# Optimization experiments

Hardware: AMD Instinct MI355X
Metric: run time of the kernel (lower is better)

Reference implementation:

```python
import jax, jax.numpy as jnp
import numpy as np

NUM_HEADS = 8
DIM = 256
NW = 64  # number of windows per batch element


def setup_inputs() -> dict:
    key = jax.random.key(0)
    k_x, k_m, k_ws, k_wm, k_wp, k_bp = jax.random.split(key, 6)
    B_, N, C = 512, 128, DIM
    x = jax.random.normal(k_x, (B_, N, C), dtype=jnp.float32)
    # 0 / -100 additive attention mask (stand-in for the 0/-inf shift-window mask)
    mask = jnp.where(jax.random.uniform(k_m, (NW, N, N)) < 0.5, 0.0, -100.0).astype(jnp.float32)
    std = 0.02
    w_qkv_self = jax.random.normal(k_ws, (3 * C, C), dtype=jnp.float32) * std
    w_qkv_mut = jax.random.normal(k_wm, (3 * C, C), dtype=jnp.float32) * std
    w_proj = jax.random.normal(k_wp, (C, 2 * C), dtype=jnp.float32) * std
    b_proj = jax.random.normal(k_bp, (C,), dtype=jnp.float32) * std
    return {"x": x, "mask": mask, "w_qkv_self": w_qkv_self,
            "w_qkv_mut": w_qkv_mut, "w_proj": w_proj, "b_proj": b_proj}


def _split_qkv(x, w):
    # x: (B_, N, C); w: (3C, C) torch Linear weight -> y = x @ w.T
    B_, N, C = x.shape
    d = C // NUM_HEADS
    qkv = (x @ w.T).reshape(B_, N, 3, NUM_HEADS, d).transpose(2, 0, 3, 1, 4)
    return qkv[0], qkv[1], qkv[2]  # each (B_, H, N, d)


def _attention(q, k, v, mask, scale):
    # q,k,v: (B_, H, n, d); mask: (nW, Nfull, Nfull) additive
    B_, H, n, d = q.shape
    nW = mask.shape[0]
    attn = jnp.einsum('bhnd,bhmd->bhnm', q * scale, k)  # (B_, H, n, n)
    attn = attn.reshape(B_ // nW, nW, H, n, n) + mask[None, :, None, :n, :n]
    attn = jax.nn.softmax(attn.reshape(B_, H, n, n), axis=-1)
    out = jnp.einsum('bhnm,bhmd->bhnd', attn, v)
    return out.transpose(0, 2, 1, 3).reshape(B_, n, H * d)  # (B_, n, C)


def reference(x, mask, w_qkv_self, w_qkv_mut, w_proj, b_proj):
    B_, N, C = x.shape
    scale = (C // NUM_HEADS) ** (-0.5)
    # self window attention
    q, k, v = _split_qkv(x, w_qkv_self)
    x_out = _attention(q, k, v, mask, scale)  # (B_, N, C)
    # mutual (cross-frame) attention between the two halves of the window
    qm, km, vm = _split_qkv(x, w_qkv_mut)
    h = N // 2
    q1, q2 = qm[:, :, :h], qm[:, :, h:]
    k1, k2 = km[:, :, :h], km[:, :, h:]
    v1, v2 = vm[:, :, :h], vm[:, :, h:]
    x1_aligned = _attention(q2, k1, v1, mask, scale)  # (B_, N//2, C)
    x2_aligned = _attention(q1, k2, v2, mask, scale)  # (B_, N//2, C)
    x_mut = jnp.concatenate([x1_aligned, x2_aligned], axis=1)  # (B_, N, C)
    x_cat = jnp.concatenate([x_mut, x_out], axis=2)  # (B_, N, 2C)
    return x_cat @ w_proj.T + b_proj  # (B_, N, C)
```

## Files before the change

### kernel.cpp

```cpp
#include <hip/hip_runtime.h>
#include <stdint.h>

typedef __bf16 bf16x4 __attribute__((ext_vector_type(4)));
typedef __bf16 bf16x8 __attribute__((ext_vector_type(8)));
typedef float f32x4 __attribute__((ext_vector_type(4)));

#define DEVI __device__ __forceinline__

DEVI ushort bfbits(float f) {
  union { __bf16 b; ushort u; } v;
  v.b = (__bf16)f;
  return v.u;
}

DEVI void gload16(const void* g, void* l) {
  auto* gp = reinterpret_cast<const __attribute__((address_space(1))) uint32_t*>(
      reinterpret_cast<uintptr_t>(g));
  auto* lp = reinterpret_cast<__attribute__((address_space(3))) uint32_t*>(
      reinterpret_cast<uintptr_t>(l));
  __builtin_amdgcn_global_load_lds(gp, lp, 16, 0, 0);
}

__global__ __launch_bounds__(256) void cvt_x(const float* __restrict__ in,
                                             ushort* __restrict__ out) {
  int i = (blockIdx.x * 256 + threadIdx.x) * 4;
  float4 v = *(const float4*)(in + i);
  ushort4 o;
  o.x = bfbits(v.x); o.y = bfbits(v.y); o.z = bfbits(v.z); o.w = bfbits(v.w);
  *(ushort4*)(out + i) = o;
}

__global__ __launch_bounds__(256) void cvt_w(const float* __restrict__ ws,
                                             const float* __restrict__ wm,
                                             const float* __restrict__ wp,
                                             ushort* __restrict__ wqkv,
                                             ushort* __restrict__ wproj) {
  int i = blockIdx.x * 256 + threadIdx.x;
  if (i < 196608)       wqkv[i] = bfbits(ws[i]);
  else if (i < 393216)  wqkv[i] = bfbits(wm[i - 196608]);
  else                  wproj[i - 393216] = bfbits(wp[i - 393216]);
}

template <int KF, int NH>
DEVI void attn_body(const ushort* Qs, const ushort* Ks, const ushort* Vt,
                    ushort* Ps, const float* mrow, ushort* ob,
                    int qrow0, int kvbase, int orow0, int mrow0,
                    int lr, int lc) {
  const float L2E = 1.4426950408889634f;

  f32x4 sacc[2][KF];
#pragma unroll
  for (int mf = 0; mf < 2; ++mf)
#pragma unroll
    for (int nf = 0; nf < KF; ++nf) sacc[mf][nf] = (f32x4){0.f, 0.f, 0.f, 0.f};

  bf16x8 aq[2];
#pragma unroll
  for (int mf = 0; mf < 2; ++mf) {
    int r = qrow0 + mf * 16 + lr;
    aq[mf] = *(const bf16x8*)(Qs + r * 32 + ((lc ^ ((r >> 1) & 3)) * 8));
  }
  __builtin_amdgcn_s_setprio(1);
#pragma unroll
  for (int nf = 0; nf < KF; ++nf) {
    int r = kvbase + nf * 16 + lr;
    bf16x8 bk = *(const bf16x8*)(Ks + r * 32 + ((lc ^ ((r >> 1) & 3)) * 8));
#pragma unroll
    for (int mf = 0; mf < 2; ++mf)
      sacc[mf][nf] = __builtin_amdgcn_mfma_f32_16x16x32_bf16(aq[mf], bk, sacc[mf][nf], 0, 0, 0);
  }
  __builtin_amdgcn_s_setprio(0);

#pragma unroll
  for (int mf = 0; mf < 2; ++mf)
#pragma unroll
    for (int nf = 0; nf < KF; ++nf)
#pragma unroll
      for (int r = 0; r < 4; ++r) {
        int row = mrow0 + mf * 16 + lc * 4 + r;
        int col = nf * 16 + lr;
        sacc[mf][nf][r] = fmaf(mrow[row * 128 + col], L2E, sacc[mf][nf][r]);
      }
  float sinv[2][4];
#pragma unroll
  for (int mf = 0; mf < 2; ++mf)
#pragma unroll
    for (int r = 0; r < 4; ++r) {
      float s = 0.f;
#pragma unroll
      for (int nf = 0; nf < KF; ++nf) {
        float e = __builtin_amdgcn_exp2f(sacc[mf][nf][r]);
        sacc[mf][nf][r] = e;
        s += e;
      }
#pragma unroll
      for (int d = 1; d < 16; d <<= 1) s += __shfl_xor(s, d);
      sinv[mf][r] = __builtin_amdgcn_rcpf(s);
    }

  f32x4 oacc[2][2];
#pragma unroll
  for (int mf = 0; mf < 2; ++mf)
#pragma unroll
    for (int nf = 0; nf < 2; ++nf) oacc[mf][nf] = (f32x4){0.f, 0.f, 0.f, 0.f};

#pragma unroll
  for (int hf = 0; hf < NH; ++hf) {
    __syncthreads();
#pragma unroll
    for (int mf = 0; mf < 2; ++mf)
#pragma unroll
      for (int r = 0; r < 4; ++r) {
        int prow = orow0 + mf * 16 + lc * 4 + r;
#pragma unroll
        for (int nf2 = 0; nf2 < 4; ++nf2) {
          int col = nf2 * 16 + lr;
          int grp = (col >> 3) ^ (prow & 7);
          Ps[prow * 64 + grp * 8 + (col & 7)] = bfbits(sacc[mf][hf * 4 + nf2][r]);
        }
      }
    __syncthreads();
    __builtin_amdgcn_s_setprio(1);
#pragma unroll
    for (int ks = 0; ks < 2; ++ks) {
      bf16x8 pf[2], vf[2];
#pragma unroll
      for (int mf = 0; mf < 2; ++mf) {
        int prow = orow0 + mf * 16 + lr;
        int grp = (ks * 4 + lc) ^ (prow & 7);
        pf[mf] = *(const bf16x8*)(Ps + prow * 64 + grp * 8);
      }
#pragma unroll
      for (int nf = 0; nf < 2; ++nf)
        vf[nf] = *(const bf16x8*)(Vt + (nf * 16 + lr) * 136 + kvbase + hf * 64 + ks * 32 + lc * 8);
#pragma unroll
      for (int mf = 0; mf < 2; ++mf)
#pragma unroll
        for (int nf = 0; nf < 2; ++nf)
          oacc[mf][nf] = __builtin_amdgcn_mfma_f32_16x16x32_bf16(pf[mf], vf[nf], oacc[mf][nf], 0, 0, 0);
    }
    __builtin_amdgcn_s_setprio(0);
  }

#pragma unroll
  for (int mf = 0; mf < 2; ++mf)
#pragma unroll
    for (int nf = 0; nf < 2; ++nf)
#pragma unroll
      for (int r = 0; r < 4; ++r) {
        int row = orow0 + mf * 16 + lc * 4 + r;
        int col = nf * 16 + lr;
        ob[(size_t)row * 512 + col] = bfbits(oacc[mf][nf][r] * sinv[mf][r]);
      }
}

__global__ __launch_bounds__(256) void attn_fused(const ushort* __restrict__ xb,
                                                  const ushort* __restrict__ wqkv,
                                                  const float* __restrict__ mask,
                                                  ushort* __restrict__ xcat) {
  __shared__ __align__(16) uint8_t smem[28672];
  ushort* xs0 = (ushort*)smem;
  ushort* wl0 = (ushort*)(smem + 8192);
  ushort* xs1 = (ushort*)(smem + 14336);
  ushort* wl1 = (ushort*)(smem + 22528);
  ushort* Qs  = (ushort*)smem;
  ushort* Ks  = (ushort*)(smem + 8192);
  ushort* Vt  = (ushort*)(smem + 16384);
  ushort* Ps  = (ushort*)smem;

  const int bid = blockIdx.x;
  const int c = bid & 7;
  const int u = bid >> 3;
  const int m = u & 1;
  const int h = (u >> 1) & 7;
  const int b = (u >> 4) * 8 + c;
  const int wmask = b & 63;
  const int t = threadIdx.x;
  const int wid = t >> 6, l = t & 63;
  const int lr = l & 15, lc = l >> 4;
  const float qscale = 0.17677669529663687f * 1.4426950408889634f;

  const ushort* xrow = xb + (size_t)b * 128 * 256;
  const int wbase = m * 768;

  auto STAGE = [&](int kk, ushort* xs, ushort* wl) {
#pragma unroll
    for (int p = 0; p < 2; ++p) {
      int slot = t + p * 256;
      int row = slot >> 2, cs = slot & 3;
      int cd = cs ^ ((row >> 1) & 3);
      gload16(xrow + (size_t)row * 256 + kk + cd * 8, xs + slot * 8);
    }
    {
      int slot = t;
      int row = slot >> 2, cs = slot & 3;
      int cd = cs ^ ((row >> 1) & 3);
      int grow = wbase + (row >> 5) * 256 + h * 32 + (row & 31);
      gload16(wqkv + (size_t)grow * 256 + kk + cd * 8, wl + slot * 8);
    }
    if (t < 128) {
      int slot = t + 256;
      int row = slot >> 2, cs = slot & 3;
      int cd = cs ^ ((row >> 1) & 3);
      int grow = wbase + (row >> 5) * 256 + h * 32 + (row & 31);
      gload16(wqkv + (size_t)grow * 256 + kk + cd * 8, wl + slot * 8);
    }
  };

  f32x4 pacc[2][6];
#pragma unroll
  for (int mf = 0; mf < 2; ++mf)
#pragma unroll
    for (int n = 0; n < 6; ++n) pacc[mf][n] = (f32x4){0.f, 0.f, 0.f, 0.f};

  STAGE(0, xs0, wl0);
#pragma unroll
  for (int k = 0; k < 8; ++k) {
    __syncthreads();
    if (k < 7) {
      if ((k & 1) == 0) STAGE((k + 1) * 32, xs1, wl1);
      else              STAGE((k + 1) * 32, xs0, wl0);
    }
    const ushort* xs = (k & 1) ? xs1 : xs0;
    const ushort* wl = (k & 1) ? wl1 : wl0;

    bf16x8 ax[2];
#pragma unroll
    for (int mf = 0; mf < 2; ++mf) {
      int r = wid * 32 + mf * 16 + lr;
      ax[mf] = *(const bf16x8*)(xs + r * 32 + ((lc ^ ((r >> 1) & 3)) * 8));
    }
    __builtin_amdgcn_s_setprio(1);
#pragma unroll
    for (int n = 0; n < 6; ++n) {
      int r = n * 16 + lr;
      bf16x8 bw = *(const bf16x8*)(wl + r * 32 + ((lc ^ ((r >> 1) & 3)) * 8));
#pragma unroll
      for (int mf = 0; mf < 2; ++mf)
        pacc[mf][n] = __builtin_amdgcn_mfma_f32_16x16x32_bf16(ax[mf], bw, pacc[mf][n], 0, 0, 0);
    }
    __builtin_amdgcn_s_setprio(0);
  }
  __syncthreads();

#pragma unroll
  for (int mf = 0; mf < 2; ++mf) {
#pragma unroll
    for (int n = 0; n < 4; ++n)
#pragma unroll
      for (int j = 0; j < 4; ++j) {
        int row = wid * 32 + mf * 16 + lc * 4 + j;
        int d = (n & 1) * 16 + lr;
        float v = pacc[mf][n][j];
        if (n < 2) v *= qscale;
        int sw = ((d >> 3) ^ ((row >> 1) & 3)) * 8 + (d & 7);
        (n < 2 ? Qs : Ks)[row * 32 + sw] = bfbits(v);
      }
#pragma unroll
    for (int k = 0; k < 2; ++k) {
      bf16x4 pk;
#pragma unroll
      for (int j = 0; j < 4; ++j) pk[j] = (__bf16)pacc[mf][4 + k][j];
      int d = k * 16 + lr;
      int row0 = wid * 32 + mf * 16 + lc * 4;
      *(bf16x4*)(Vt + d * 136 + row0) = pk;
    }
  }
  __syncthreads();

  const float* mrow = mask + (size_t)wmask * 16384;

  if (m == 0) {
    ushort* ob = xcat + (size_t)b * 128 * 512 + 256 + h * 32;
    attn_body<8, 2>(Qs, Ks, Vt, Ps, mrow, ob,
                    wid * 32, 0,
                    wid * 32, wid * 32, lr, lc);
  } else {
    const int half = wid >> 1, sub = wid & 1;
    ushort* ob = xcat + (size_t)b * 128 * 512 + h * 32;
    attn_body<4, 1>(Qs, Ks, Vt, Ps, mrow, ob,
                    (half ? 0 : 64) + sub * 32, half ? 64 : 0,
                    half * 64 + sub * 32, sub * 32, lr, lc);
  }
}

__global__ __launch_bounds__(256) void gemm_proj(const ushort* __restrict__ A,
                                                 const ushort* __restrict__ B,
                                                 const float* __restrict__ bias,
                                                 float* __restrict__ out) {
  __shared__ ushort As[64 * 32];
  __shared__ ushort Bs[256 * 32];
  const int t = threadIdx.x, tm = blockIdx.x;
  const int w = t >> 6, l = t & 63;
  const int wc = w * 64;
  const int lr = l & 15, lc = l >> 4;
  const ushort* Ab = A + (size_t)tm * 64 * 512;

  f32x4 acc[4][4];
#pragma unroll
  for (int m = 0; m < 4; ++m)
#pragma unroll
    for (int n = 0; n < 4; ++n) acc[m][n] = (f32x4){0.f, 0.f, 0.f, 0.f};

  for (int kk = 0; kk < 512; kk += 32) {
    __syncthreads();
    {
      int slot = t;
      int row = slot >> 2, cs = slot & 3;
      int cd = cs ^ ((row >> 1) & 3);
      gload16(Ab + (size_t)row * 512 + kk + cd * 8, As + slot * 8);
    }
#pragma unroll
    for (int p = 0; p < 4; ++p) {
      int slot = t + p * 256;
      int row = slot >> 2, cs = slot & 3;
      int cd = cs ^ ((row >> 1) & 3);
      gload16(B + (size_t)row * 512 + kk + cd * 8, Bs + slot * 8);
    }
    __syncthreads();

    bf16x8 af[4], bfr[4];
#pragma unroll
    for (int m = 0; m < 4; ++m) {
      int r = m * 16 + lr;
      af[m] = *(const bf16x8*)(As + r * 32 + ((lc ^ ((r >> 1) & 3)) * 8));
    }
#pragma unroll
    for (int n = 0; n < 4; ++n) {
      int r = wc + n * 16 + lr;
      bfr[n] = *(const bf16x8*)(Bs + r * 32 + ((lc ^ ((r >> 1) & 3)) * 8));
    }
    __builtin_amdgcn_s_setprio(1);
#pragma unroll
    for (int m = 0; m < 4; ++m)
#pragma unroll
      for (int n = 0; n < 4; ++n)
        acc[m][n] = __builtin_amdgcn_mfma_f32_16x16x32_bf16(af[m], bfr[n], acc[m][n], 0, 0, 0);
    __builtin_amdgcn_s_setprio(0);
  }

#pragma unroll
  for (int m = 0; m < 4; ++m)
#pragma unroll
    for (int n = 0; n < 4; ++n)
#pragma unroll
      for (int r = 0; r < 4; ++r) {
        int row = tm * 64 + m * 16 + lc * 4 + r;
        int col = wc + n * 16 + lr;
        out[(size_t)row * 256 + col] = acc[m][n][r] + bias[col];
      }
}

extern "C" void kernel_launch(void* const* d_in, const int* in_sizes, int n_in,
                              void* d_out, int out_size, void* d_ws, size_t ws_size,
                              hipStream_t stream) {
  const float* x = (const float*)d_in[0];
  const float* mask = (const float*)d_in[1];
  const float* w_qkv_self = (const float*)d_in[2];
  const float* w_qkv_mut = (const float*)d_in[3];
  const float* w_proj = (const float*)d_in[4];
  const float* b_proj = (const float*)d_in[5];
  float* out = (float*)d_out;

  uint8_t* ws = (uint8_t*)d_ws;
  ushort* xb    = (ushort*)(ws);
  ushort* wqkv  = (ushort*)(ws + 33554432);
  ushort* wproj = (ushort*)(ws + 34340864);
  ushort* xcat  = (ushort*)d_out;

  cvt_x<<<dim3(16384), dim3(256), 0, stream>>>(x, xb);
  cvt_w<<<dim3(2048), dim3(256), 0, stream>>>(w_qkv_self, w_qkv_mut, w_proj, wqkv, wproj);
  attn_fused<<<dim3(8192), dim3(256), 0, stream>>>(xb, wqkv, mask, xcat);
  gemm_proj<<<dim3(1024), dim3(256), 0, stream>>>(xcat, wproj, b_proj, out);
}
```

Before: 178.7 us.

## Transpose score MFMA so mask loads vectorize and row sums need fewer shuffles

The QK^T MFMA now runs with swapped operands, so each lane holds four consecutive key columns for one query row. That lets the additive mask be read as float4 vectors, cuts the row-sum reduction to two cross-lane shuffles, and lets P be written to LDS as packed bf16x4 into a padded (stride 72) layout instead of a XOR swizzle. Because the output accumulator layout no longer matches the row-sum owner, the reciprocal sums are staged through a new LDS array. Vt and the LDS map are shifted to make room, which adds shared-memory traffic and relies on the new offsets not overlapping live buffers.

```diff
diff --git a/kernel.cpp b/kernel.cpp
--- a/kernel.cpp
+++ b/kernel.cpp
@@ -43,115 +43,115 @@
 
 template <int KF, int NH>
 DEVI void attn_body(const ushort* Qs, const ushort* Ks, const ushort* Vt,
-                    ushort* Ps, const float* mrow, ushort* ob,
+                    ushort* Ps, float* sinvs, const float* mrow, ushort* ob,
                     int qrow0, int kvbase, int orow0, int mrow0,
                     int lr, int lc) {
   const float L2E = 1.4426950408889634f;
 
-  f32x4 sacc[2][KF];
-#pragma unroll
-  for (int mf = 0; mf < 2; ++mf)
-#pragma unroll
-    for (int nf = 0; nf < KF; ++nf) sacc[mf][nf] = (f32x4){0.f, 0.f, 0.f, 0.f};
+  f32x4 sacc[KF][2];
+#pragma unroll
+  for (int kf = 0; kf < KF; ++kf)
+#pragma unroll
+    for (int tf = 0; tf < 2; ++tf) sacc[kf][tf] = (f32x4){0.f, 0.f, 0.f, 0.f};
 
   bf16x8 aq[2];
 #pragma unroll
-  for (int mf = 0; mf < 2; ++mf) {
-    int r = qrow0 + mf * 16 + lr;
-    aq[mf] = *(const bf16x8*)(Qs + r * 32 + ((lc ^ ((r >> 1) & 3)) * 8));
+  for (int tf = 0; tf < 2; ++tf) {
+    int r = qrow0 + tf * 16 + lr;
+    aq[tf] = *(const bf16x8*)(Qs + r * 32 + ((lc ^ ((r >> 1) & 3)) * 8));
   }
   __builtin_amdgcn_s_setprio(1);
 #pragma unroll
-  for (int nf = 0; nf < KF; ++nf) {
-    int r = kvbase + nf * 16 + lr;
+  for (int kf = 0; kf < KF; ++kf) {
+    int r = kvbase + kf * 16 + lr;
     bf16x8 bk = *(const bf16x8*)(Ks + r * 32 + ((lc ^ ((r >> 1) & 3)) * 8));
 #pragma unroll
-    for (int mf = 0; mf < 2; ++mf)
-      sacc[mf][nf] = __builtin_amdgcn_mfma_f32_16x16x32_bf16(aq[mf], bk, sacc[mf][nf], 0, 0, 0);
+    for (int tf = 0; tf < 2; ++tf)
+      sacc[kf][tf] = __builtin_amdgcn_mfma_f32_16x16x32_bf16(bk, aq[tf], sacc[kf][tf], 0, 0, 0);
   }
   __builtin_amdgcn_s_setprio(0);
 
 #pragma unroll
-  for (int mf = 0; mf < 2; ++mf)
-#pragma unroll
-    for (int nf = 0; nf < KF; ++nf)
+  for (int tf = 0; tf < 2; ++tf) {
+    const float* mtok = mrow + (size_t)(mrow0 + tf * 16 + lr) * 128;
+#pragma unroll
+    for (int kf = 0; kf < KF; ++kf) {
+      f32x4 mv = *(const f32x4*)(mtok + kf * 16 + lc * 4);
+#pragma unroll
+      for (int r = 0; r < 4; ++r)
+        sacc[kf][tf][r] = fmaf(mv[r], L2E, sacc[kf][tf][r]);
+    }
+  }
+
+#pragma unroll
+  for (int tf = 0; tf < 2; ++tf) {
+    float s = 0.f;
+#pragma unroll
+    for (int kf = 0; kf < KF; ++kf)
 #pragma unroll
       for (int r = 0; r < 4; ++r) {
-        int row = mrow0 + mf * 16 + lc * 4 + r;
-        int col = nf * 16 + lr;
-        sacc[mf][nf][r] = fmaf(mrow[row * 128 + col], L2E, sacc[mf][nf][r]);
-      }
-  float sinv[2][4];
-#pragma unroll
-  for (int mf = 0; mf < 2; ++mf)
-#pragma unroll
-    for (int r = 0; r < 4; ++r) {
-      float s = 0.f;
-#pragma unroll
-      for (int nf = 0; nf < KF; ++nf) {
-        float e = __builtin_amdgcn_exp2f(sacc[mf][nf][r]);
-        sacc[mf][nf][r] = e;
+        float e = __builtin_amdgcn_exp2f(sacc[kf][tf][r]);
+        sacc[kf][tf][r] = e;
         s += e;
       }
-#pragma unroll
-      for (int d = 1; d < 16; d <<= 1) s += __shfl_xor(s, d);
-      sinv[mf][r] = __builtin_amdgcn_rcpf(s);
-    }
+    s += __shfl_xor(s, 16);
+    s += __shfl_xor(s, 32);
+    sinvs[orow0 + tf * 16 + lr] = __builtin_amdgcn_rcpf(s);
+  }
 
   f32x4 oacc[2][2];
 #pragma unroll
-  for (int mf = 0; mf < 2; ++mf)
-#pragma unroll
-    for (int nf = 0; nf < 2; ++nf) oacc[mf][nf] = (f32x4){0.f, 0.f, 0.f, 0.f};
+  for (int tf = 0; tf < 2; ++tf)
+#pragma unroll
+    for (int nd = 0; nd < 2; ++nd) oacc[tf][nd] = (f32x4){0.f, 0.f, 0.f, 0.f};
 
 #pragma unroll
   for (int hf = 0; hf < NH; ++hf) {
     __syncthreads();
 #pragma unroll
-    for (int mf = 0; mf < 2; ++mf)
-#pragma unroll
-      for (int r = 0; r < 4; ++r) {
-        int prow = orow0 + mf * 16 + lc * 4 + r;
-#pragma unroll
-        for (int nf2 = 0; nf2 < 4; ++nf2) {
-          int col = nf2 * 16 + lr;
-          int grp = (col >> 3) ^ (prow & 7);
-          Ps[prow * 64 + grp * 8 + (col & 7)] = bfbits(sacc[mf][hf * 4 + nf2][r]);
-        }
-      }
+    for (int tf = 0; tf < 2; ++tf) {
+      int tok = orow0 + tf * 16 + lr;
+#pragma unroll
+      for (int kf4 = 0; kf4 < 4; ++kf4) {
+        f32x4 v = sacc[hf * 4 + kf4][tf];
+        bf16x4 pk;
+#pragma unroll
+        for (int j = 0; j < 4; ++j) pk[j] = (__bf16)v[j];
+        *(bf16x4*)(Ps + tok * 72 + kf4 * 16 + lc * 4) = pk;
+      }
+    }
     __syncthreads();
     __builtin_amdgcn_s_setprio(1);
 #pragma unroll
     for (int ks = 0; ks < 2; ++ks) {
       bf16x8 pf[2], vf[2];
 #pragma unroll
-      for (int mf = 0; mf < 2; ++mf) {
-        int prow = orow0 + mf * 16 + lr;
-        int grp = (ks * 4 + lc) ^ (prow & 7);
-        pf[mf] = *(const bf16x8*)(Ps + prow * 64 + grp * 8);
-      }
-#pragma unroll
-      for (int nf = 0; nf < 2; ++nf)
-        vf[nf] = *(const bf16x8*)(Vt + (nf * 16 + lr) * 136 + kvbase + hf * 64 + ks * 32 + lc * 8);
-#pragma unroll
-      for (int mf = 0; mf < 2; ++mf)
-#pragma unroll
-        for (int nf = 0; nf < 2; ++nf)
-          oacc[mf][nf] = __builtin_amdgcn_mfma_f32_16x16x32_bf16(pf[mf], vf[nf], oacc[mf][nf], 0, 0, 0);
+      for (int tf = 0; tf < 2; ++tf)
+        pf[tf] = *(const bf16x8*)(Ps + (orow0 + tf * 16 + lr) * 72 + ks * 32 + lc * 8);
+#pragma unroll
+      for (int nd = 0; nd < 2; ++nd)
+        vf[nd] = *(const bf16x8*)(Vt + (nd * 16 + lr) * 136 + kvbase + hf * 64 + ks * 32 + lc * 8);
+#pragma unroll
+      for (int tf = 0; tf < 2; ++tf)
+#pragma unroll
+        for (int nd = 0; nd < 2; ++nd)
+          oacc[tf][nd] = __builtin_amdgcn_mfma_f32_16x16x32_bf16(pf[tf], vf[nd], oacc[tf][nd], 0, 0, 0);
     }
     __builtin_amdgcn_s_setprio(0);
   }
 
 #pragma unroll
-  for (int mf = 0; mf < 2; ++mf)
-#pragma unroll
-    for (int nf = 0; nf < 2; ++nf)
+  for (int tf = 0; tf < 2; ++tf) {
+    f32x4 sv = *(const f32x4*)(sinvs + orow0 + tf * 16 + lc * 4);
+#pragma unroll
+    for (int nd = 0; nd < 2; ++nd)
 #pragma unroll
       for (int r = 0; r < 4; ++r) {
-        int row = orow0 + mf * 16 + lc * 4 + r;
-        int col = nf * 16 + lr;
-        ob[(size_t)row * 512 + col] = bfbits(oacc[mf][nf][r] * sinv[mf][r]);
-      }
+        int row = orow0 + tf * 16 + lc * 4 + r;
+        int col = nd * 16 + lr;
+        ob[(size_t)row * 512 + col] = bfbits(oacc[tf][nd][r] * sv[r]);
+      }
+  }
 }
 
 __global__ __launch_bounds__(256) void attn_fused(const ushort* __restrict__ xb,
@@ -163,10 +163,11 @@
   ushort* wl0 = (ushort*)(smem + 8192);
   ushort* xs1 = (ushort*)(smem + 14336);
   ushort* wl1 = (ushort*)(smem + 22528);
-  ushort* Qs  = (ushort*)smem;
-  ushort* Ks  = (ushort*)(smem + 8192);
-  ushort* Vt  = (ushort*)(smem + 16384);
-  ushort* Ps  = (ushort*)smem;
+  ushort* Qs    = (ushort*)smem;
+  ushort* Ks    = (ushort*)(smem + 8192);
+  ushort* Vt    = (ushort*)(smem + 18432);
+  float*  sinvs = (float*)(smem + 27136);
+  ushort* Ps    = (ushort*)smem;
 
   const int bid = blockIdx.x;
   const int c = bid & 7;
@@ -272,13 +273,13 @@
 
   if (m == 0) {
     ushort* ob = xcat + (size_t)b * 128 * 512 + 256 + h * 32;
-    attn_body<8, 2>(Qs, Ks, Vt, Ps, mrow, ob,
+    attn_body<8, 2>(Qs, Ks, Vt, Ps, sinvs, mrow, ob,
                     wid * 32, 0,
                     wid * 32, wid * 32, lr, lc);
   } else {
     const int half = wid >> 1, sub = wid & 1;
     ushort* ob = xcat + (size_t)b * 128 * 512 + h * 32;
-    attn_body<4, 1>(Qs, Ks, Vt, Ps, mrow, ob,
+    attn_body<4, 1>(Qs, Ks, Vt, Ps, sinvs, mrow, ob,
                     (half ? 0 : 64) + sub * 32, half ? 64 : 0,
                     half * 64 + sub * 32, sub * 32, lr, lc);
   }
```

After: 194.1 us. +8.6%, slower.
